# Kernel tuning notes

Measured on AMD Instinct MI355X. Metric: run time of the kernel, lower is better.

## Reference

```python
import jax, jax.numpy as jnp
import numpy as np

N_NODES = 50000
N_EDGES = 800000
D = 64
P = 2.0  # init kwarg p


def setup_inputs() -> dict:
    key = jax.random.key(0)
    k1, k2, k3, k4 = jax.random.split(key, 4)
    X = jax.random.normal(k1, (N_NODES, D), dtype=jnp.float32)
    edge_index = jax.random.randint(k2, (2, N_EDGES), 0, N_NODES, dtype=jnp.int64)
    # SAGEConv params (Glorot-ish scale)
    s = 1.0 / np.sqrt(D)
    W_neigh = jax.random.normal(k3, (D, D), dtype=jnp.float32) * s
    W_self = jax.random.normal(k4, (D, D), dtype=jnp.float32) * s
    b = jnp.zeros((D,), dtype=jnp.float32)
    return {"X": X, "edge_index": edge_index, "W_neigh": W_neigh, "W_self": W_self, "b": b}


def _segment_mean(vals, idx, num_segments):
    # vals: [E, D], idx: [E] -> [num_segments, D]; mean with empty segments = 0
    s = jax.ops.segment_sum(vals, idx, num_segments=num_segments)
    cnt = jax.ops.segment_sum(jnp.ones((vals.shape[0],), vals.dtype), idx,
                              num_segments=num_segments)
    return s / jnp.maximum(cnt, 1.0)[:, None]


def reference(X, edge_index, W_neigh, W_self, b):
    src = edge_index[0]
    dst = edge_index[1]
    n = X.shape[0]
    # SAGEConv (mean aggregation): messages X[src] aggregated at dst
    agg = _segment_mean(X[src], dst, n)                      # [N, D]
    h = jax.nn.relu(agg @ W_neigh + X @ W_self + b)          # [N, D]
    # edge gather, |diff|^p, scatter-mean to src nodes, tanh
    m = jnp.abs(h[src] - h[dst]) ** P                        # [E, D]
    gg = jnp.tanh(_segment_mean(m, src, n))                  # [N, D]
    return gg
```

## Files before the change

### kernel.cpp

```cpp
#include <hip/hip_runtime.h>
#include <math.h>

#define D 64
#define SCAN_ELEMS 1024
#define STEP 256
#define SHIFT 8
#define PART_CHUNK 2048


typedef __attribute__((ext_vector_type(8))) short bf16x8;
typedef __attribute__((ext_vector_type(8))) unsigned short u16x8;
typedef __attribute__((ext_vector_type(4))) float f32x4;

__device__ inline unsigned short f2bf(float f) {
    unsigned u = __float_as_uint(f);
    return (unsigned short)((u + 0x7FFFu + ((u >> 16) & 1u)) >> 16);
}
__device__ inline float bf2f(unsigned short h) {
    return __uint_as_float(((unsigned)h) << 16);
}

__global__ __launch_bounds__(256) void to_bf16(
    const float* __restrict__ in, unsigned short* __restrict__ outh, int n8) {
    int i = blockIdx.x * blockDim.x + threadIdx.x;
    if (i >= n8) return;
    const float4* p = (const float4*)in + (size_t)i * 2;
    float4 a = p[0], b = p[1];
    union { unsigned short us[8]; uint4 v; } u;
    u.us[0] = f2bf(a.x); u.us[1] = f2bf(a.y); u.us[2] = f2bf(a.z); u.us[3] = f2bf(a.w);
    u.us[4] = f2bf(b.x); u.us[5] = f2bf(b.y); u.us[6] = f2bf(b.z); u.us[7] = f2bf(b.w);
    ((uint4*)outh)[i] = u.v;
}

__global__ __launch_bounds__(256) void part_hist(
    const int* __restrict__ src, const int* __restrict__ dst,
    int* __restrict__ cnt, int nE, int nN, int K, int WGs) {
    __shared__ int lh[1024];
    int wg = blockIdx.x;
    for (int i = threadIdx.x; i < K; i += 256) lh[i] = 0;
    __syncthreads();
    int base = wg * PART_CHUNK;
    int lim = min(base + PART_CHUNK, nE);
    for (int e = base + threadIdx.x; e < lim; e += 256) {
        int s = src[e], t = dst[e];
        atomicAdd(&lh[t >> SHIFT], 1);
        atomicAdd(&lh[(nN + s) >> SHIFT], 1);
    }
    __syncthreads();
    for (int b = threadIdx.x; b < K; b += 256) cnt[b * WGs + wg] = lh[b];
}

__global__ __launch_bounds__(256) void scan_part(
    const int* __restrict__ in, int* __restrict__ bsum, int n) {
    __shared__ int sdata[256];
    int b = blockIdx.x, t = threadIdx.x;
    int base = b * SCAN_ELEMS + t * 4;
    int s = 0;
#pragma unroll
    for (int k = 0; k < 4; ++k) { int i = base + k; if (i < n) s += in[i]; }
    sdata[t] = s;
    __syncthreads();
    for (int o = 128; o > 0; o >>= 1) {
        if (t < o) sdata[t] += sdata[t + o];
        __syncthreads();
    }
    if (t == 0) bsum[b] = sdata[0];
}

__global__ __launch_bounds__(256) void scan_tops(int* __restrict__ bsum, int nb) {
    __shared__ int sd[256];
    int t = threadIdx.x;
    int v = (t < nb) ? bsum[t] : 0;
    sd[t] = v;
    __syncthreads();
    for (int o = 1; o < 256; o <<= 1) {
        int u = (t >= o) ? sd[t - o] : 0;
        __syncthreads();
        sd[t] += u;
        __syncthreads();
    }
    if (t < nb) bsum[t] = sd[t] - v;
}

__global__ __launch_bounds__(256) void scan_final(
    const int* __restrict__ in, const int* __restrict__ bsum,
    int* __restrict__ out, int n) {
    __shared__ int sth[256];
    int b = blockIdx.x, t = threadIdx.x;
    int base = b * SCAN_ELEMS + t * 4;
    int v[4]; int s = 0;
#pragma unroll
    for (int k = 0; k < 4; ++k) { int i = base + k; v[k] = (i < n) ? in[i] : 0; s += v[k]; }
    sth[t] = s;
    __syncthreads();
    for (int o = 1; o < 256; o <<= 1) {
        int u = (t >= o) ? sth[t - o] : 0;
        __syncthreads();
        sth[t] += u;
        __syncthreads();
    }
    int run = sth[t] - s + bsum[b];
#pragma unroll
    for (int k = 0; k < 4; ++k) {
        int i = base + k;
        if (i < n) { out[i] = run; run += v[k]; }
    }
}

__global__ __launch_bounds__(256) void part_write(
    const int* __restrict__ src, const int* __restrict__ dst,
    const int* __restrict__ scanned, unsigned int* __restrict__ part,
    int nE, int nN, int K, int WGs) {
    __shared__ int cur[1024];
    int wg = blockIdx.x;
    for (int b = threadIdx.x; b < K; b += 256) cur[b] = scanned[b * WGs + wg];
    __syncthreads();
    int base = wg * PART_CHUNK;
    int lim = min(base + PART_CHUNK, nE);
    for (int e = base + threadIdx.x; e < lim; e += 256) {
        int s = src[e], t = dst[e];
        int k1 = t;
        int p1 = atomicAdd(&cur[k1 >> SHIFT], 1);
        part[p1] = ((unsigned)(k1 & (STEP - 1)) << 16) | (unsigned)s;
        int k2 = nN + s;
        int p2 = atomicAdd(&cur[k2 >> SHIFT], 1);
        part[p2] = ((unsigned)(k2 & (STEP - 1)) << 16) | (unsigned)t;
    }
}

__global__ __launch_bounds__(256) void csr_build(
    const unsigned int* __restrict__ part, const int* __restrict__ scanned,
    unsigned short* __restrict__ vals, int* __restrict__ off,
    int n2, int K, int WGs, int totalItems) {
    __shared__ int deg[STEP];
    __shared__ int pfx[STEP];
    int b = blockIdx.x, t = threadIdx.x;
    int base = scanned[b * WGs];
    int endi = (b + 1 < K) ? scanned[(b + 1) * WGs] : totalItems;

    deg[t] = 0;
    __syncthreads();
    for (int i = base + t; i < endi; i += 256)
        atomicAdd(&deg[part[i] >> 16], 1);
    __syncthreads();

    pfx[t] = deg[t];
    __syncthreads();
    for (int o = 1; o < STEP; o <<= 1) {
        int u = (t >= o) ? pfx[t - o] : 0;
        __syncthreads();
        pfx[t] += u;
        __syncthreads();
    }
    int ex = pfx[t] - deg[t];
    int g = b * STEP + t;
    if (g < n2) off[g] = base + ex;
    if (b == K - 1 && t == 0) off[n2] = totalItems;
    deg[t] = ex;
    __syncthreads();

    for (int i = base + t; i < endi; i += 256) {
        unsigned u = part[i];
        int l = (int)(u >> 16);
        int p = atomicAdd(&deg[l], 1);
        vals[base + p] = (unsigned short)(u & 0xffffu);
    }
}

#define ANODES 8
#define ROWB 144
__global__ __launch_bounds__(512) void agg_gemm(
    const unsigned short* __restrict__ Xh,
    const int* __restrict__ off,
    const unsigned short* __restrict__ vals,
    const unsigned short* __restrict__ Whn,
    const unsigned short* __restrict__ Whs,
    const float* __restrict__ bias,
    unsigned short* __restrict__ hh, int nNodes) {
    __shared__ __align__(16) unsigned short rows[2][16][72];

    int t = threadIdx.x;
    if (t < 288) {
        int b = t / 144, r = t - b * 144;
        *(unsigned long long*)((char*)&rows[b][8][0] + r * 8) = 0ULL;
    }

    int li = t >> 6;
    int lane = t & 63;
    int g = lane >> 3;
    int q = lane & 7;
    int bb = blockIdx.x * ANODES;
    int node = bb + li;

    float acc[8];
#pragma unroll
    for (int j = 0; j < 8; ++j) acc[j] = 0.f;

    int beg = 0, end = 0;
    if (node < nNodes) { beg = off[node]; end = off[node + 1]; }

    int base = beg;
    for (; base + 16 <= end; base += 16) {
        int s0 = vals[base + g];
        int s1 = vals[base + 8 + g];
        u16x8 v0 = ((const u16x8*)(Xh + (size_t)s0 * D))[q];
        u16x8 v1 = ((const u16x8*)(Xh + (size_t)s1 * D))[q];
#pragma unroll
        for (int j = 0; j < 8; ++j) acc[j] += bf2f(v0[j]) + bf2f(v1[j]);
    }
    for (; base + 8 <= end; base += 8) {
        int s0 = vals[base + g];
        u16x8 v0 = ((const u16x8*)(Xh + (size_t)s0 * D))[q];
#pragma unroll
        for (int j = 0; j < 8; ++j) acc[j] += bf2f(v0[j]);
    }
    int rem = end - base;
    if (g < rem) {
        int s0 = vals[base + g];
        u16x8 v0 = ((const u16x8*)(Xh + (size_t)s0 * D))[q];
#pragma unroll
        for (int j = 0; j < 8; ++j) acc[j] += bf2f(v0[j]);
    }
#pragma unroll
    for (int j = 0; j < 8; ++j) {
        acc[j] += __shfl_xor(acc[j], 8);
        acc[j] += __shfl_xor(acc[j], 16);
        acc[j] += __shfl_xor(acc[j], 32);
    }

    if (node < nNodes && g == 0) {
        float inv = 1.0f / fmaxf((float)(end - beg), 1.0f);
        u16x8 mv;
#pragma unroll
        for (int j = 0; j < 8; ++j) mv[j] = f2bf(acc[j] * inv);
        *(u16x8*)((char*)&rows[0][li][0] + q * 16) = mv;
        u16x8 xv = ((const u16x8*)(Xh + (size_t)node * D))[q];
        *(u16x8*)((char*)&rows[1][li][0] + q * 16) = xv;
    }
    __syncthreads();

    if (li >= 4) return;
    int c = lane & 15;
    int hi = lane >> 4;
    f32x4 accm;
    float bv = bias[li * 16 + c];
    accm[0] = bv; accm[1] = bv; accm[2] = bv; accm[3] = bv;
#pragma unroll
    for (int kh = 0; kh < 2; ++kh) {
        bf16x8 aA = *(const bf16x8*)((const char*)&rows[0][0][0] + c * ROWB + kh * 64 + hi * 16);
        bf16x8 aX = *(const bf16x8*)((const char*)&rows[1][0][0] + c * ROWB + kh * 64 + hi * 16);
        bf16x8 bN, bS;
        int kb = kh * 32 + hi * 8;
#pragma unroll
        for (int j = 0; j < 8; ++j) {
            bN[j] = (short)Whn[(size_t)(kb + j) * D + li * 16 + c];
            bS[j] = (short)Whs[(size_t)(kb + j) * D + li * 16 + c];
        }
        accm = __builtin_amdgcn_mfma_f32_16x16x32_bf16(aA, bN, accm, 0, 0, 0);
        accm = __builtin_amdgcn_mfma_f32_16x16x32_bf16(aX, bS, accm, 0, 0, 0);
    }
#pragma unroll
    for (int r = 0; r < 4; ++r) {
        int row = hi * 4 + r;
        if (row < 8) {
            int n2a = bb + row;
            if (n2a < nNodes)
                hh[(size_t)n2a * D + li * 16 + c] = f2bf(fmaxf(accm[r], 0.0f));
        }
    }
}

__global__ __launch_bounds__(256) void m_gather(
    const unsigned short* __restrict__ hh,
    const int* __restrict__ off,
    const unsigned short* __restrict__ vals,
    float* __restrict__ out, int nNodes) {
    int t = threadIdx.x;
    int li = t >> 6;
    int lane = t & 63;
    int g = lane >> 3;
    int q = lane & 7;
    int node = blockIdx.x * 4 + li;
    if (node >= nNodes) return;

    u16x8 hv = ((const u16x8*)(hh + (size_t)node * D))[q];
    float hn[8];
#pragma unroll
    for (int j = 0; j < 8; ++j) hn[j] = bf2f(hv[j]);

    int beg = off[nNodes + node];
    int end = off[nNodes + node + 1];

    float acc[8];
#pragma unroll
    for (int j = 0; j < 8; ++j) acc[j] = 0.f;

    int base = beg;
    for (; base + 16 <= end; base += 16) {
        int t0 = vals[base + g];
        int t1 = vals[base + 8 + g];
        u16x8 u0 = ((const u16x8*)(hh + (size_t)t0 * D))[q];
        u16x8 u1 = ((const u16x8*)(hh + (size_t)t1 * D))[q];
#pragma unroll
        for (int j = 0; j < 8; ++j) {
            float d0 = hn[j] - bf2f(u0[j]);
            float d1 = hn[j] - bf2f(u1[j]);
            acc[j] += d0 * d0 + d1 * d1;
        }
    }
    for (; base + 8 <= end; base += 8) {
        int t0 = vals[base + g];
        u16x8 u0 = ((const u16x8*)(hh + (size_t)t0 * D))[q];
#pragma unroll
        for (int j = 0; j < 8; ++j) {
            float d0 = hn[j] - bf2f(u0[j]);
            acc[j] += d0 * d0;
        }
    }
    int rem = end - base;
    if (g < rem) {
        int t0 = vals[base + g];
        u16x8 u0 = ((const u16x8*)(hh + (size_t)t0 * D))[q];
#pragma unroll
        for (int j = 0; j < 8; ++j) {
            float d0 = hn[j] - bf2f(u0[j]);
            acc[j] += d0 * d0;
        }
    }
#pragma unroll
    for (int j = 0; j < 8; ++j) {
        acc[j] += __shfl_xor(acc[j], 8);
        acc[j] += __shfl_xor(acc[j], 16);
        acc[j] += __shfl_xor(acc[j], 32);
    }

    if (g == 0) {
        float inv = 1.0f / fmaxf((float)(end - beg), 1.0f);
        float4 r0, r1;
        r0.x = tanhf(acc[0] * inv); r0.y = tanhf(acc[1] * inv);
        r0.z = tanhf(acc[2] * inv); r0.w = tanhf(acc[3] * inv);
        r1.x = tanhf(acc[4] * inv); r1.y = tanhf(acc[5] * inv);
        r1.z = tanhf(acc[6] * inv); r1.w = tanhf(acc[7] * inv);
        ((float4*)(out + (size_t)node * D))[q * 2] = r0;
        ((float4*)(out + (size_t)node * D))[q * 2 + 1] = r1;
    }
}

extern "C" void kernel_launch(void* const* d_in, const int* in_sizes, int n_in,
                              void* d_out, int out_size, void* d_ws, size_t ws_size,
                              hipStream_t stream) {
    const float* X  = (const float*)d_in[0];
    const int*   ei = (const int*)d_in[1];
    const float* Wn = (const float*)d_in[2];
    const float* Ws = (const float*)d_in[3];
    const float* b  = (const float*)d_in[4];
    float* out = (float*)d_out;

    int nNodes = in_sizes[0] / D;
    int nEdges = in_sizes[1] / 2;
    const int* src = ei;
    const int* dst = ei + nEdges;

    int n2 = 2 * nNodes;
    int K = (n2 + STEP - 1) / STEP;
    int WGs = (nEdges + PART_CHUNK - 1) / PART_CHUNK;
    int nCnt = K * WGs;
    int nb = (nCnt + SCAN_ELEMS - 1) / SCAN_ELEMS;
    int totalItems = 2 * nEdges;

    size_t o = 0;
    auto align4 = [](size_t x) { return (x + 3) & ~(size_t)3; };
    int* cnt     = (int*)d_ws;                 o = align4((size_t)nCnt);
    int* scanned = (int*)d_ws + o;             o = align4(o + (size_t)nCnt);
    int* bsum    = (int*)d_ws + o;             o = align4(o + 256);
    int* off     = (int*)d_ws + o;             o = align4(o + (size_t)n2 + 1);
    unsigned int* part = (unsigned int*)((int*)d_ws + o);
    o = align4(o + 2 * (size_t)nEdges);
    unsigned short* vals = (unsigned short*)((int*)d_ws + o);
    o = align4(o + (size_t)nEdges);
    unsigned short* Xh = (unsigned short*)((int*)d_ws + o);
    o = align4(o + (size_t)nNodes * D / 2);
    unsigned short* hh = (unsigned short*)((int*)d_ws + o);
    o = align4(o + (size_t)nNodes * D / 2);
    unsigned short* Whn = (unsigned short*)((int*)d_ws + o);
    o = align4(o + (size_t)(D * D) / 2);
    unsigned short* Whs = (unsigned short*)((int*)d_ws + o);

    int n8 = nNodes * D / 8;
    to_bf16<<<(n8 + 255) / 256, 256, 0, stream>>>(X, Xh, n8);
    to_bf16<<<2, 256, 0, stream>>>(Wn, Whn, D * D / 8);
    to_bf16<<<2, 256, 0, stream>>>(Ws, Whs, D * D / 8);

    part_hist<<<WGs, 256, 0, stream>>>(src, dst, cnt, nEdges, nNodes, K, WGs);
    scan_part<<<nb, 256, 0, stream>>>(cnt, bsum, nCnt);
    scan_tops<<<1, 256, 0, stream>>>(bsum, nb);
    scan_final<<<nb, 256, 0, stream>>>(cnt, bsum, scanned, nCnt);
    part_write<<<WGs, 256, 0, stream>>>(src, dst, scanned, part, nEdges, nNodes, K, WGs);
    csr_build<<<K, STEP, 0, stream>>>(part, scanned, vals, off, n2, K, WGs, totalItems);

    int aBlocks = (nNodes + ANODES - 1) / ANODES;
    agg_gemm<<<aBlocks, 512, 0, stream>>>(Xh, off, vals, Whn, Whs, b, hh, nNodes);
    int mBlocks = (nNodes + 3) / 4;
    m_gather<<<mBlocks, 256, 0, stream>>>(hh, off, vals, out, nNodes);
}
```

Measured before the change: 116.1 us.

## Split gathers into column-half passes and separate aggregation from GEMM

After: 156.5 us. 1.35x slower.

```diff
diff --git a/kernel.cpp b/kernel.cpp
--- a/kernel.cpp
+++ b/kernel.cpp
@@ -20,16 +20,23 @@
     return __uint_as_float(((unsigned)h) << 16);
 }
 
-__global__ __launch_bounds__(256) void to_bf16(
-    const float* __restrict__ in, unsigned short* __restrict__ outh, int n8) {
+__global__ __launch_bounds__(256) void to_bf16_all(
+    const float* __restrict__ X, const float* __restrict__ Wn,
+    const float* __restrict__ Ws, unsigned short* __restrict__ Xh,
+    unsigned short* __restrict__ Whn, unsigned short* __restrict__ Whs,
+    int n8x, int n8w) {
     int i = blockIdx.x * blockDim.x + threadIdx.x;
-    if (i >= n8) return;
-    const float4* p = (const float4*)in + (size_t)i * 2;
+    const float* in; unsigned short* outh; int idx;
+    if (i < n8x) { in = X; outh = Xh; idx = i; }
+    else if (i < n8x + n8w) { in = Wn; outh = Whn; idx = i - n8x; }
+    else if (i < n8x + 2 * n8w) { in = Ws; outh = Whs; idx = i - n8x - n8w; }
+    else return;
+    const float4* p = (const float4*)in + (size_t)idx * 2;
     float4 a = p[0], b = p[1];
     union { unsigned short us[8]; uint4 v; } u;
     u.us[0] = f2bf(a.x); u.us[1] = f2bf(a.y); u.us[2] = f2bf(a.z); u.us[3] = f2bf(a.w);
     u.us[4] = f2bf(b.x); u.us[5] = f2bf(b.y); u.us[6] = f2bf(b.z); u.us[7] = f2bf(b.w);
-    ((uint4*)outh)[i] = u.v;
+    ((uint4*)outh)[idx] = u.v;
 }
 
 __global__ __launch_bounds__(256) void part_hist(
@@ -167,123 +174,121 @@
     }
 }
 
-#define ANODES 8
-#define ROWB 144
-__global__ __launch_bounds__(512) void agg_gemm(
+__global__ __launch_bounds__(256) void agg_mean_half(
     const unsigned short* __restrict__ Xh,
     const int* __restrict__ off,
     const unsigned short* __restrict__ vals,
+    unsigned short* __restrict__ Am,
+    int nNodes, int half) {
+    int t = threadIdx.x;
+    int li = t >> 6;
+    int lane = t & 63;
+    int g = lane >> 2;
+    int q = lane & 3;
+    int node = blockIdx.x * 4 + li;
+    if (node >= nNodes) return;
+
+    const unsigned short* tab = Xh + half * 32 + 8 * q;
+    int beg = off[node], end = off[node + 1];
+
+    float acc[8];
+#pragma unroll
+    for (int j = 0; j < 8; ++j) acc[j] = 0.f;
+
+    int base = beg;
+    for (; base + 32 <= end; base += 32) {
+        int s0 = vals[base + g];
+        int s1 = vals[base + 16 + g];
+        u16x8 v0 = *(const u16x8*)(tab + (size_t)s0 * D);
+        u16x8 v1 = *(const u16x8*)(tab + (size_t)s1 * D);
+#pragma unroll
+        for (int j = 0; j < 8; ++j) acc[j] += bf2f(v0[j]) + bf2f(v1[j]);
+    }
+    for (; base + 16 <= end; base += 16) {
+        int s0 = vals[base + g];
+        u16x8 v0 = *(const u16x8*)(tab + (size_t)s0 * D);
+#pragma unroll
+        for (int j = 0; j < 8; ++j) acc[j] += bf2f(v0[j]);
+    }
+    int rem = end - base;
+    if (g < rem) {
+        int s0 = vals[base + g];
+        u16x8 v0 = *(const u16x8*)(tab + (size_t)s0 * D);
+#pragma unroll
+        for (int j = 0; j < 8; ++j) acc[j] += bf2f(v0[j]);
+    }
+#pragma unroll
+    for (int j = 0; j < 8; ++j) {
+        acc[j] += __shfl_xor(acc[j], 4);
+        acc[j] += __shfl_xor(acc[j], 8);
+        acc[j] += __shfl_xor(acc[j], 16);
+        acc[j] += __shfl_xor(acc[j], 32);
+    }
+
+    if (g == 0) {
+        float inv = 1.0f / fmaxf((float)(end - beg), 1.0f);
+        u16x8 mv;
+#pragma unroll
+        for (int j = 0; j < 8; ++j) mv[j] = f2bf(acc[j] * inv);
+        *(u16x8*)(Am + (size_t)node * D + half * 32 + 8 * q) = mv;
+    }
+}
+
+__global__ __launch_bounds__(256) void gemm_h(
+    const unsigned short* __restrict__ Am,
+    const unsigned short* __restrict__ Xh,
     const unsigned short* __restrict__ Whn,
     const unsigned short* __restrict__ Whs,
     const float* __restrict__ bias,
     unsigned short* __restrict__ hh, int nNodes) {
-    __shared__ __align__(16) unsigned short rows[2][16][72];
-
     int t = threadIdx.x;
-    if (t < 288) {
-        int b = t / 144, r = t - b * 144;
-        *(unsigned long long*)((char*)&rows[b][8][0] + r * 8) = 0ULL;
-    }
-
-    int li = t >> 6;
+    int w = t >> 6;
     int lane = t & 63;
-    int g = lane >> 3;
-    int q = lane & 7;
-    int bb = blockIdx.x * ANODES;
-    int node = bb + li;
-
-    float acc[8];
-#pragma unroll
-    for (int j = 0; j < 8; ++j) acc[j] = 0.f;
-
-    int beg = 0, end = 0;
-    if (node < nNodes) { beg = off[node]; end = off[node + 1]; }
-
-    int base = beg;
-    for (; base + 16 <= end; base += 16) {
-        int s0 = vals[base + g];
-        int s1 = vals[base + 8 + g];
-        u16x8 v0 = ((const u16x8*)(Xh + (size_t)s0 * D))[q];
-        u16x8 v1 = ((const u16x8*)(Xh + (size_t)s1 * D))[q];
-#pragma unroll
-        for (int j = 0; j < 8; ++j) acc[j] += bf2f(v0[j]) + bf2f(v1[j]);
-    }
-    for (; base + 8 <= end; base += 8) {
-        int s0 = vals[base + g];
-        u16x8 v0 = ((const u16x8*)(Xh + (size_t)s0 * D))[q];
-#pragma unroll
-        for (int j = 0; j < 8; ++j) acc[j] += bf2f(v0[j]);
-    }
-    int rem = end - base;
-    if (g < rem) {
-        int s0 = vals[base + g];
-        u16x8 v0 = ((const u16x8*)(Xh + (size_t)s0 * D))[q];
-#pragma unroll
-        for (int j = 0; j < 8; ++j) acc[j] += bf2f(v0[j]);
-    }
-#pragma unroll
-    for (int j = 0; j < 8; ++j) {
-        acc[j] += __shfl_xor(acc[j], 8);
-        acc[j] += __shfl_xor(acc[j], 16);
-        acc[j] += __shfl_xor(acc[j], 32);
-    }
-
-    if (node < nNodes && g == 0) {
-        float inv = 1.0f / fmaxf((float)(end - beg), 1.0f);
-        u16x8 mv;
-#pragma unroll
-        for (int j = 0; j < 8; ++j) mv[j] = f2bf(acc[j] * inv);
-        *(u16x8*)((char*)&rows[0][li][0] + q * 16) = mv;
-        u16x8 xv = ((const u16x8*)(Xh + (size_t)node * D))[q];
-        *(u16x8*)((char*)&rows[1][li][0] + q * 16) = xv;
-    }
-    __syncthreads();
-
-    if (li >= 4) return;
     int c = lane & 15;
     int hi = lane >> 4;
-    f32x4 accm;
-    float bv = bias[li * 16 + c];
-    accm[0] = bv; accm[1] = bv; accm[2] = bv; accm[3] = bv;
+    int nb = blockIdx.x * 16;
+    int arow = min(nb + c, nNodes - 1);
+
+    f32x4 acc;
+    float bv = bias[w * 16 + c];
+    acc[0] = bv; acc[1] = bv; acc[2] = bv; acc[3] = bv;
 #pragma unroll
     for (int kh = 0; kh < 2; ++kh) {
-        bf16x8 aA = *(const bf16x8*)((const char*)&rows[0][0][0] + c * ROWB + kh * 64 + hi * 16);
-        bf16x8 aX = *(const bf16x8*)((const char*)&rows[1][0][0] + c * ROWB + kh * 64 + hi * 16);
+        bf16x8 aA = *(const bf16x8*)(Am + (size_t)arow * D + kh * 32 + hi * 8);
+        bf16x8 aX = *(const bf16x8*)(Xh + (size_t)arow * D + kh * 32 + hi * 8);
         bf16x8 bN, bS;
         int kb = kh * 32 + hi * 8;
 #pragma unroll
         for (int j = 0; j < 8; ++j) {
-            bN[j] = (short)Whn[(size_t)(kb + j) * D + li * 16 + c];
-            bS[j] = (short)Whs[(size_t)(kb + j) * D + li * 16 + c];
+            bN[j] = (short)Whn[(size_t)(kb + j) * D + w * 16 + c];
+            bS[j] = (short)Whs[(size_t)(kb + j) * D + w * 16 + c];
         }
-        accm = __builtin_amdgcn_mfma_f32_16x16x32_bf16(aA, bN, accm, 0, 0, 0);
-        accm = __builtin_amdgcn_mfma_f32_16x16x32_bf16(aX, bS, accm, 0, 0, 0);
+        acc = __builtin_amdgcn_mfma_f32_16x16x32_bf16(aA, bN, acc, 0, 0, 0);
+        acc = __builtin_amdgcn_mfma_f32_16x16x32_bf16(aX, bS, acc, 0, 0, 0);
     }
 #pragma unroll
     for (int r = 0; r < 4; ++r) {
-        int row = hi * 4 + r;
-        if (row < 8) {
-            int n2a = bb + row;
-            if (n2a < nNodes)
-                hh[(size_t)n2a * D + li * 16 + c] = f2bf(fmaxf(accm[r], 0.0f));
-        }
-    }
-}
-
-__global__ __launch_bounds__(256) void m_gather(
+        int node = nb + hi * 4 + r;
+        if (node < nNodes)
+            hh[(size_t)node * D + w * 16 + c] = f2bf(fmaxf(acc[r], 0.0f));
+    }
+}
+
+__global__ __launch_bounds__(256) void m_half(
     const unsigned short* __restrict__ hh,
     const int* __restrict__ off,
     const unsigned short* __restrict__ vals,
-    float* __restrict__ out, int nNodes) {
+    float* __restrict__ out, int nNodes, int half) {
     int t = threadIdx.x;
     int li = t >> 6;
     int lane = t & 63;
-    int g = lane >> 3;
-    int q = lane & 7;
+    int g = lane >> 2;
+    int q = lane & 3;
     int node = blockIdx.x * 4 + li;
     if (node >= nNodes) return;
 
-    u16x8 hv = ((const u16x8*)(hh + (size_t)node * D))[q];
+    const unsigned short* tab = hh + half * 32 + 8 * q;
+    u16x8 hv = *(const u16x8*)(tab + (size_t)node * D);
     float hn[8];
 #pragma unroll
     for (int j = 0; j < 8; ++j) hn[j] = bf2f(hv[j]);
@@ -296,11 +301,11 @@
     for (int j = 0; j < 8; ++j) acc[j] = 0.f;
 
     int base = beg;
-    for (; base + 16 <= end; base += 16) {
+    for (; base + 32 <= end; base += 32) {
         int t0 = vals[base + g];
-        int t1 = vals[base + 8 + g];
-        u16x8 u0 = ((const u16x8*)(hh + (size_t)t0 * D))[q];
-        u16x8 u1 = ((const u16x8*)(hh + (size_t)t1 * D))[q];
+        int t1 = vals[base + 16 + g];
+        u16x8 u0 = *(const u16x8*)(tab + (size_t)t0 * D);
+        u16x8 u1 = *(const u16x8*)(tab + (size_t)t1 * D);
 #pragma unroll
         for (int j = 0; j < 8; ++j) {
             float d0 = hn[j] - bf2f(u0[j]);
@@ -308,9 +313,9 @@
             acc[j] += d0 * d0 + d1 * d1;
         }
     }
-    for (; base + 8 <= end; base += 8) {
+    for (; base + 16 <= end; base += 16) {
         int t0 = vals[base + g];
-        u16x8 u0 = ((const u16x8*)(hh + (size_t)t0 * D))[q];
+        u16x8 u0 = *(const u16x8*)(tab + (size_t)t0 * D);
 #pragma unroll
         for (int j = 0; j < 8; ++j) {
             float d0 = hn[j] - bf2f(u0[j]);
@@ -320,7 +325,7 @@
     int rem = end - base;
     if (g < rem) {
         int t0 = vals[base + g];
-        u16x8 u0 = ((const u16x8*)(hh + (size_t)t0 * D))[q];
+        u16x8 u0 = *(const u16x8*)(tab + (size_t)t0 * D);
 #pragma unroll
         for (int j = 0; j < 8; ++j) {
             float d0 = hn[j] - bf2f(u0[j]);
@@ -329,6 +334,7 @@
     }
 #pragma unroll
     for (int j = 0; j < 8; ++j) {
+        acc[j] += __shfl_xor(acc[j], 4);
         acc[j] += __shfl_xor(acc[j], 8);
         acc[j] += __shfl_xor(acc[j], 16);
         acc[j] += __shfl_xor(acc[j], 32);
@@ -336,13 +342,14 @@
 
     if (g == 0) {
         float inv = 1.0f / fmaxf((float)(end - beg), 1.0f);
+        float* po = out + (size_t)node * D + half * 32 + 8 * q;
         float4 r0, r1;
         r0.x = tanhf(acc[0] * inv); r0.y = tanhf(acc[1] * inv);
         r0.z = tanhf(acc[2] * inv); r0.w = tanhf(acc[3] * inv);
         r1.x = tanhf(acc[4] * inv); r1.y = tanhf(acc[5] * inv);
         r1.z = tanhf(acc[6] * inv); r1.w = tanhf(acc[7] * inv);
-        ((float4*)(out + (size_t)node * D))[q * 2] = r0;
-        ((float4*)(out + (size_t)node * D))[q * 2 + 1] = r1;
+        ((float4*)po)[0] = r0;
+        ((float4*)po)[1] = r1;
     }
 }
 
@@ -382,14 +389,16 @@
     o = align4(o + (size_t)nNodes * D / 2);
     unsigned short* hh = (unsigned short*)((int*)d_ws + o);
     o = align4(o + (size_t)nNodes * D / 2);
+    unsigned short* Am = (unsigned short*)((int*)d_ws + o);
+    o = align4(o + (size_t)nNodes * D / 2);
     unsigned short* Whn = (unsigned short*)((int*)d_ws + o);
     o = align4(o + (size_t)(D * D) / 2);
     unsigned short* Whs = (unsigned short*)((int*)d_ws + o);
 
-    int n8 = nNodes * D / 8;
-    to_bf16<<<(n8 + 255) / 256, 256, 0, stream>>>(X, Xh, n8);
-    to_bf16<<<2, 256, 0, stream>>>(Wn, Whn, D * D / 8);
-    to_bf16<<<2, 256, 0, stream>>>(Ws, Whs, D * D / 8);
+    int n8x = nNodes * D / 8;
+    int n8w = D * D / 8;
+    int cvtBlocks = (n8x + 2 * n8w + 255) / 256;
+    to_bf16_all<<<cvtBlocks, 256, 0, stream>>>(X, Wn, Ws, Xh, Whn, Whs, n8x, n8w);
 
     part_hist<<<WGs, 256, 0, stream>>>(src, dst, cnt, nEdges, nNodes, K, WGs);
     scan_part<<<nb, 256, 0, stream>>>(cnt, bsum, nCnt);
@@ -398,8 +407,13 @@
     part_write<<<WGs, 256, 0, stream>>>(src, dst, scanned, part, nEdges, nNodes, K, WGs);
     csr_build<<<K, STEP, 0, stream>>>(part, scanned, vals, off, n2, K, WGs, totalItems);
 
-    int aBlocks = (nNodes + ANODES - 1) / ANODES;
-    agg_gemm<<<aBlocks, 512, 0, stream>>>(Xh, off, vals, Whn, Whs, b, hh, nNodes);
-    int mBlocks = (nNodes + 3) / 4;
-    m_gather<<<mBlocks, 256, 0, stream>>>(hh, off, vals, out, nNodes);
-}
+    int gBlocks = (nNodes + 3) / 4;
+    agg_mean_half<<<gBlocks, 256, 0, stream>>>(Xh, off, vals, Am, nNodes, 0);
+    agg_mean_half<<<gBlocks, 256, 0, stream>>>(Xh, off, vals, Am, nNodes, 1);
+
+    int hBlocks = (nNodes + 15) / 16;
+    gemm_h<<<hBlocks, 256, 0, stream>>>(Am, Xh, Whn, Whs, b, hh, nNodes);
+
+    m_half<<<gBlocks, 256, 0, stream>>>(hh, off, vals, out, nNodes, 0);
+    m_half<<<gBlocks, 256, 0, stream>>>(hh, off, vals, out, nNodes, 1);
+}
```

## Fuse bf16 conversions into histogram launch and halve wave width per node in m_gather

Applied to the files above, without the earlier changes.

After: 106.3 us. 1.09x faster.

```diff
diff --git a/kernel.cpp b/kernel.cpp
--- a/kernel.cpp
+++ b/kernel.cpp
@@ -20,23 +20,30 @@
     return __uint_as_float(((unsigned)h) << 16);
 }
 
-__global__ __launch_bounds__(256) void to_bf16(
-    const float* __restrict__ in, unsigned short* __restrict__ outh, int n8) {
-    int i = blockIdx.x * blockDim.x + threadIdx.x;
-    if (i >= n8) return;
-    const float4* p = (const float4*)in + (size_t)i * 2;
-    float4 a = p[0], b = p[1];
-    union { unsigned short us[8]; uint4 v; } u;
-    u.us[0] = f2bf(a.x); u.us[1] = f2bf(a.y); u.us[2] = f2bf(a.z); u.us[3] = f2bf(a.w);
-    u.us[4] = f2bf(b.x); u.us[5] = f2bf(b.y); u.us[6] = f2bf(b.z); u.us[7] = f2bf(b.w);
-    ((uint4*)outh)[i] = u.v;
-}
-
-__global__ __launch_bounds__(256) void part_hist(
+__global__ __launch_bounds__(256) void part_hist_cvt(
     const int* __restrict__ src, const int* __restrict__ dst,
-    int* __restrict__ cnt, int nE, int nN, int K, int WGs) {
+    int* __restrict__ cnt, int nE, int nN, int K, int WGs,
+    const float* __restrict__ X, const float* __restrict__ Wn,
+    const float* __restrict__ Ws, unsigned short* __restrict__ Xh,
+    unsigned short* __restrict__ Whn, unsigned short* __restrict__ Whs,
+    int n8x, int n8w) {
     __shared__ int lh[1024];
     int wg = blockIdx.x;
+    if (wg >= WGs) {
+        int i = (wg - WGs) * 256 + threadIdx.x;
+        const float* in; unsigned short* outh; int idx;
+        if (i < n8x) { in = X; outh = Xh; idx = i; }
+        else if (i < n8x + n8w) { in = Wn; outh = Whn; idx = i - n8x; }
+        else if (i < n8x + 2 * n8w) { in = Ws; outh = Whs; idx = i - n8x - n8w; }
+        else return;
+        const float4* p = (const float4*)in + (size_t)idx * 2;
+        float4 a = p[0], b = p[1];
+        union { unsigned short us[8]; uint4 v; } u;
+        u.us[0] = f2bf(a.x); u.us[1] = f2bf(a.y); u.us[2] = f2bf(a.z); u.us[3] = f2bf(a.w);
+        u.us[4] = f2bf(b.x); u.us[5] = f2bf(b.y); u.us[6] = f2bf(b.z); u.us[7] = f2bf(b.w);
+        ((uint4*)outh)[idx] = u.v;
+        return;
+    }
     for (int i = threadIdx.x; i < K; i += 256) lh[i] = 0;
     __syncthreads();
     int base = wg * PART_CHUNK;
@@ -276,20 +283,24 @@
     const unsigned short* __restrict__ vals,
     float* __restrict__ out, int nNodes) {
     int t = threadIdx.x;
-    int li = t >> 6;
+    int w = t >> 6;
     int lane = t & 63;
-    int g = lane >> 3;
+    int half = lane >> 5;
+    int gg = (lane >> 3) & 3;
     int q = lane & 7;
-    int node = blockIdx.x * 4 + li;
-    if (node >= nNodes) return;
-
-    u16x8 hv = ((const u16x8*)(hh + (size_t)node * D))[q];
+    int node = blockIdx.x * 8 + w * 2 + half;
+    bool valid = node < nNodes;
+
+    u16x8 hv = {};
+    int beg = 0, end = 0;
+    if (valid) {
+        hv = ((const u16x8*)(hh + (size_t)node * D))[q];
+        beg = off[nNodes + node];
+        end = off[nNodes + node + 1];
+    }
     float hn[8];
 #pragma unroll
     for (int j = 0; j < 8; ++j) hn[j] = bf2f(hv[j]);
-
-    int beg = off[nNodes + node];
-    int end = off[nNodes + node + 1];
 
     float acc[8];
 #pragma unroll
@@ -297,19 +308,25 @@
 
     int base = beg;
     for (; base + 16 <= end; base += 16) {
-        int t0 = vals[base + g];
-        int t1 = vals[base + 8 + g];
+        int t0 = vals[base + gg];
+        int t1 = vals[base + 4 + gg];
+        int t2 = vals[base + 8 + gg];
+        int t3 = vals[base + 12 + gg];
         u16x8 u0 = ((const u16x8*)(hh + (size_t)t0 * D))[q];
         u16x8 u1 = ((const u16x8*)(hh + (size_t)t1 * D))[q];
+        u16x8 u2 = ((const u16x8*)(hh + (size_t)t2 * D))[q];
+        u16x8 u3 = ((const u16x8*)(hh + (size_t)t3 * D))[q];
 #pragma unroll
         for (int j = 0; j < 8; ++j) {
             float d0 = hn[j] - bf2f(u0[j]);
             float d1 = hn[j] - bf2f(u1[j]);
-            acc[j] += d0 * d0 + d1 * d1;
+            float d2 = hn[j] - bf2f(u2[j]);
+            float d3 = hn[j] - bf2f(u3[j]);
+            acc[j] += d0 * d0 + d1 * d1 + d2 * d2 + d3 * d3;
         }
     }
-    for (; base + 8 <= end; base += 8) {
-        int t0 = vals[base + g];
+    for (; base + 4 <= end; base += 4) {
+        int t0 = vals[base + gg];
         u16x8 u0 = ((const u16x8*)(hh + (size_t)t0 * D))[q];
 #pragma unroll
         for (int j = 0; j < 8; ++j) {
@@ -318,8 +335,8 @@
         }
     }
     int rem = end - base;
-    if (g < rem) {
-        int t0 = vals[base + g];
+    if (gg < rem) {
+        int t0 = vals[base + gg];
         u16x8 u0 = ((const u16x8*)(hh + (size_t)t0 * D))[q];
 #pragma unroll
         for (int j = 0; j < 8; ++j) {
@@ -331,10 +348,9 @@
     for (int j = 0; j < 8; ++j) {
         acc[j] += __shfl_xor(acc[j], 8);
         acc[j] += __shfl_xor(acc[j], 16);
-        acc[j] += __shfl_xor(acc[j], 32);
-    }
-
-    if (g == 0) {
+    }
+
+    if (valid && gg == 0) {
         float inv = 1.0f / fmaxf((float)(end - beg), 1.0f);
         float4 r0, r1;
         r0.x = tanhf(acc[0] * inv); r0.y = tanhf(acc[1] * inv);
@@ -386,12 +402,13 @@
     o = align4(o + (size_t)(D * D) / 2);
     unsigned short* Whs = (unsigned short*)((int*)d_ws + o);
 
-    int n8 = nNodes * D / 8;
-    to_bf16<<<(n8 + 255) / 256, 256, 0, stream>>>(X, Xh, n8);
-    to_bf16<<<2, 256, 0, stream>>>(Wn, Whn, D * D / 8);
-    to_bf16<<<2, 256, 0, stream>>>(Ws, Whs, D * D / 8);
-
-    part_hist<<<WGs, 256, 0, stream>>>(src, dst, cnt, nEdges, nNodes, K, WGs);
+    int n8x = nNodes * D / 8;
+    int n8w = D * D / 8;
+    int cvtBlocks = (n8x + 2 * n8w + 255) / 256;
+
+    part_hist_cvt<<<WGs + cvtBlocks, 256, 0, stream>>>(
+        src, dst, cnt, nEdges, nNodes, K, WGs,
+        X, Wn, Ws, Xh, Whn, Whs, n8x, n8w);
     scan_part<<<nb, 256, 0, stream>>>(cnt, bsum, nCnt);
     scan_tops<<<1, 256, 0, stream>>>(bsum, nb);
     scan_final<<<nb, 256, 0, stream>>>(cnt, bsum, scanned, nCnt);
@@ -400,6 +417,6 @@
 
     int aBlocks = (nNodes + ANODES - 1) / ANODES;
     agg_gemm<<<aBlocks, 512, 0, stream>>>(Xh, off, vals, Whn, Whs, b, hh, nNodes);
-    int mBlocks = (nNodes + 3) / 4;
+    int mBlocks = (nNodes + 7) / 8;
     m_gather<<<mBlocks, 256, 0, stream>>>(hh, off, vals, out, nNodes);
 }
```
